# Kernel tuning notes

Hardware: AMD Instinct MI355X
Metric: run time of the kernel (lower is better)

The kernel has to match this reference:

```python
import jax, jax.numpy as jnp
import numpy as np


def _conv3x3(x, w, b):
    # x: [B,C,H,W], w: [O,C,3,3], b: [O]; stride 1, padding 1 (SAME)
    y = jax.lax.conv_general_dilated(
        x, w,
        window_strides=(1, 1),
        padding=((1, 1), (1, 1)),
        dimension_numbers=("NCHW", "OIHW", "NCHW"),
    )
    return y + b[None, :, None, None]


def setup_inputs() -> dict:
    key = jax.random.key(0)
    k_x, k_w1, k_b1, k_w2, k_b2 = jax.random.split(key, 5)
    B, Cin, H, W = 16, 128, 96, 96
    Ch = 256
    # Kaiming-ish small init for conv weights
    x = jax.random.normal(k_x, (B, Cin, H, W), dtype=jnp.float32)
    w1 = jax.random.normal(k_w1, (Ch, Cin, 3, 3), dtype=jnp.float32) * (1.0 / np.sqrt(Cin * 9))
    b1 = jax.random.normal(k_b1, (Ch,), dtype=jnp.float32) * 0.01
    w2 = jax.random.normal(k_w2, (2, Ch, 3, 3), dtype=jnp.float32) * (1.0 / np.sqrt(Ch * 9))
    b2 = jax.random.normal(k_b2, (2,), dtype=jnp.float32) * 0.01
    return {"x": x, "w1": w1, "b1": b1, "w2": w2, "b2": b2}


def reference(x, w1, b1, w2, b2):
    # DeformConv2d with zero offsets == plain 3x3 conv (stride 1, pad 1) + bias.
    h = jax.nn.relu(_conv3x3(x, w1, b1))  # [B,256,H,W]
    return _conv3x3(h, w2, b2)            # [B,2,H,W]
```

## Files before the change

### kernel.cpp

```cpp
#include <hip/hip_runtime.h>
#include <stdint.h>

typedef unsigned short ushort_t;
typedef __attribute__((ext_vector_type(8))) short short8;
typedef __attribute__((ext_vector_type(4))) float floatx4;
typedef __attribute__((ext_vector_type(4))) unsigned short ushortx4;
typedef __attribute__((ext_vector_type(8))) unsigned short ushortx8;

#define B_   16
#define CIN  128
#define CH   256
#define HW   96
#define HP   98

#define XPAD_ELEMS (B_*HP*HP*CIN)
#define HPAD_ELEMS (B_*HP*HP*CH)
#define XPAD_OFF 0
#define HPAD_OFF (XPAD_ELEMS*2)
#define W1T_OFF  (HPAD_OFF + HPAD_ELEMS*2)
#define W2T_OFF  (W1T_OFF + 256*1152*2)

__device__ __forceinline__ ushort_t f2bf(float f){
  uint32_t u = __float_as_uint(f);
  u += 0x7FFF + ((u >> 16) & 1);
  return (ushort_t)(u >> 16);
}
__device__ __forceinline__ float bf2f(ushort_t h){
  return __uint_as_float(((uint32_t)h) << 16);
}
__device__ __forceinline__ void async_ld16(void* lds, const void* g){
  __builtin_amdgcn_global_load_lds(
      (const __attribute__((address_space(1))) void*)g,
      (__attribute__((address_space(3))) void*)lds, 16, 0, 0);
}

__device__ __forceinline__ void zb(uint32_t* base, int C2, int tid){
  int perimg = 388*C2;
  int b = tid / perimg; int r = tid % perimg;
  int cell = r / C2;    int cu = r % C2;
  int y, x;
  if      (cell < 98)  { y = 0;            x = cell;       }
  else if (cell < 196) { y = 97;           x = cell - 98;  }
  else if (cell < 292) { y = cell - 195;   x = 0;          }
  else                 { y = cell - 291;   x = 97;         }
  base[((b*HP + y)*HP + x)*C2 + cu] = 0u;
}

__global__ __launch_bounds__(256) void prep_all(const float* __restrict__ x,
                                                const float* __restrict__ w1,
                                                const float* __restrict__ w2,
                                                uint32_t* __restrict__ xpadw,
                                                uint32_t* __restrict__ hpadw,
                                                ushort_t* __restrict__ w1t,
                                                float* __restrict__ w2t,
                                                ushort_t* __restrict__ xpad){
  __shared__ float lds[128][33];
  int bidx = blockIdx.x;
  int t = threadIdx.x;
  if (bidx < 4608){
    int xt = bidx % 3; int y = (bidx/3) % 96; int b = bidx/288;
    int x0 = xt*32;
    #pragma unroll
    for (int rep=0; rep<16; ++rep){
      int idx = rep*256 + t;
      int ci = idx >> 5, xj = idx & 31;
      lds[ci][xj] = x[((b*CIN + ci)*HW + y)*HW + x0 + xj];
    }
    __syncthreads();
    int px = t & 31, oc = t >> 5;
    ushort_t* dst = &xpad[((b*HP + y+1)*HP + x0+px+1)*CIN + oc*16];
    ushortx8 v0, v1;
    #pragma unroll
    for (int k=0;k<8;k++) v0[k] = f2bf(lds[oc*16+k][px]);
    #pragma unroll
    for (int k=0;k<8;k++) v1[k] = f2bf(lds[oc*16+8+k][px]);
    *(ushortx8*)dst = v0;
    *(ushortx8*)(dst+8) = v1;
  } else {
    int tid = (bidx - 4608)*256 + t;
    const int NZX = B_*388*64;
    const int NZH = B_*388*128;
    const int NW1 = 256*1152;
    if (tid < NZX){
      zb(xpadw, 64, tid);
    } else if (tid < NZX + NZH){
      zb(hpadw, 128, tid - NZX);
    } else if (tid < NZX + NZH + NW1){
      int r = tid - (NZX + NZH);
      int o = r / 1152, k = r - o*1152;
      int tap = k >> 7, c = k & 127;
      w1t[r] = f2bf(w1[(o*CIN + c)*9 + tap]);
    } else {
      int r = tid - (NZX + NZH + NW1);
      int ch = r & 1, c = (r >> 1) & 255, tap = r >> 9;
      w2t[r] = w2[(ch*CH + c)*9 + tap];
    }
  }
}

#define C1_TILE(KT, VMN, SA, SB) { \
  asm volatile("s_waitcnt vmcnt(" #VMN ")" ::: "memory"); \
  __builtin_amdgcn_s_barrier(); \
  __builtin_amdgcn_sched_barrier(0); \
  const int kt_ = (KT); \
  const ushort_t* Ab = &Alds[(kt_ & 1) * 16384]; \
  const ushort_t* Bb = &Blds[(kt_ % 3) * 12288]; \
  short8 a0[4], a1[4], b0[3], b1[3], b2[3], b3[3]; \
   \
  _Pragma("unroll") \
  for (int nf=0; nf<3; ++nf) b0[nf] = *(const short8*)&Bb[bbase_r + nf*1024 + koff0]; \
  _Pragma("unroll") \
  for (int mf=0; mf<4; ++mf) a0[mf] = *(const short8*)&Ab[abase_r + mf*1024 + koff0]; \
   \
  _Pragma("unroll") \
  for (int nf=0; nf<3; ++nf) b1[nf] = *(const short8*)&Bb[bbase_r + (nf+3)*1024 + koff0]; \
  if (SA) { \
    const int ka_ = kt_ + 1; const int ab_ = (ka_ & 1) * 16384; \
    async_ld16(&Alds[ab_ +     0 + adst], &w1t[asrc +       0 + ka_*64]); \
    async_ld16(&Alds[ab_ +  4096 + adst], &w1t[asrc +   73728 + ka_*64]); \
  } \
  __builtin_amdgcn_s_barrier(); \
  __builtin_amdgcn_sched_barrier(0); \
  __builtin_amdgcn_s_setprio(1); \
  _Pragma("unroll") \
  for (int mf=0; mf<4; ++mf) \
    _Pragma("unroll") \
    for (int nf=0; nf<3; ++nf) \
      acc[mf][nf] = __builtin_amdgcn_mfma_f32_16x16x32_bf16(a0[mf], b0[nf], acc[mf][nf], 0,0,0); \
  __builtin_amdgcn_s_setprio(0); \
  __builtin_amdgcn_s_barrier(); \
  __builtin_amdgcn_sched_barrier(0); \
   \
  _Pragma("unroll") \
  for (int mf=0; mf<4; ++mf) a1[mf] = *(const short8*)&Ab[abase_r + mf*1024 + koff1]; \
  _Pragma("unroll") \
  for (int nf=0; nf<3; ++nf) b2[nf] = *(const short8*)&Bb[bbase_r + nf*1024 + koff1]; \
  if (SA) { \
    const int ka_ = kt_ + 1; const int ab_ = (ka_ & 1) * 16384; \
    async_ld16(&Alds[ab_ +  8192 + adst], &w1t[asrc + 2*73728 + ka_*64]); \
    async_ld16(&Alds[ab_ + 12288 + adst], &w1t[asrc + 3*73728 + ka_*64]); \
  } \
  __builtin_amdgcn_s_barrier(); \
  __builtin_amdgcn_sched_barrier(0); \
  __builtin_amdgcn_s_setprio(1); \
  _Pragma("unroll") \
  for (int mf=0; mf<4; ++mf) \
    _Pragma("unroll") \
    for (int nf=0; nf<3; ++nf) \
      acc[mf][nf+3] = __builtin_amdgcn_mfma_f32_16x16x32_bf16(a0[mf], b1[nf], acc[mf][nf+3], 0,0,0); \
  __builtin_amdgcn_s_setprio(0); \
  __builtin_amdgcn_s_barrier(); \
  __builtin_amdgcn_sched_barrier(0); \
   \
  _Pragma("unroll") \
  for (int nf=0; nf<3; ++nf) b3[nf] = *(const short8*)&Bb[bbase_r + (nf+3)*1024 + koff1]; \
  if (SB) { \
    const int kb_ = kt_ + 2; \
    const int tapb_ = kb_ >> 1; \
    const int dyb_ = tapb_/3; const int dxb_ = tapb_ - dyb_*3; \
    const int bdb_ = (dyb_*HP + dxb_)*CIN + (kb_&1)*64; \
    const int bb_ = (kb_ % 3) * 12288; \
    async_ld16(&Blds[bb_ +    0 + bdst], &xpad[bsrc +            bdb_]); \
    async_ld16(&Blds[bb_ + 4096 + bdst], &xpad[bsrc + 2*HP*CIN + bdb_]); \
  } \
  __builtin_amdgcn_s_barrier(); \
  __builtin_amdgcn_sched_barrier(0); \
  __builtin_amdgcn_s_setprio(1); \
  _Pragma("unroll") \
  for (int mf=0; mf<4; ++mf) \
    _Pragma("unroll") \
    for (int nf=0; nf<3; ++nf) \
      acc[mf][nf] = __builtin_amdgcn_mfma_f32_16x16x32_bf16(a1[mf], b2[nf], acc[mf][nf], 0,0,0); \
  __builtin_amdgcn_s_setprio(0); \
  __builtin_amdgcn_s_barrier(); \
  __builtin_amdgcn_sched_barrier(0); \
   \
  if (SB) { \
    const int kb_ = kt_ + 2; \
    const int tapb_ = kb_ >> 1; \
    const int dyb_ = tapb_/3; const int dxb_ = tapb_ - dyb_*3; \
    const int bdb_ = (dyb_*HP + dxb_)*CIN + (kb_&1)*64; \
    const int bb_ = (kb_ % 3) * 12288; \
    async_ld16(&Blds[bb_ + 8192 + bdst], &xpad[bsrc + 4*HP*CIN + bdb_]); \
  } \
  __builtin_amdgcn_s_barrier(); \
  __builtin_amdgcn_sched_barrier(0); \
  __builtin_amdgcn_s_setprio(1); \
  _Pragma("unroll") \
  for (int mf=0; mf<4; ++mf) \
    _Pragma("unroll") \
    for (int nf=0; nf<3; ++nf) \
      acc[mf][nf+3] = __builtin_amdgcn_mfma_f32_16x16x32_bf16(a1[mf], b3[nf], acc[mf][nf+3], 0,0,0); \
  __builtin_amdgcn_s_setprio(0); \
}

__global__ __launch_bounds__(512, 1) void conv1(const ushort_t* __restrict__ xpad,
                                                const ushort_t* __restrict__ w1t,
                                                const float* __restrict__ b1,
                                                ushort_t* __restrict__ hpad){
  __shared__ __align__(16) ushort_t Alds[2*16384];
  __shared__ __align__(16) ushort_t Blds[3*12288];
  int orig = blockIdx.x;
  int bid = (orig & 7) * 96 + (orig >> 3);
  int b = bid / 48; int rem = bid - b*48;
  int y0 = (rem/3)*6, x0 = (rem - (rem/3)*3)*32;
  int t = threadIdx.x;
  int lane = t & 63, wave = t >> 6;
  int wm = wave & 3, wn = wave >> 2;
  int r = lane & 15, q = lane >> 4;

  const int arow0 = t >> 3;
  const int soct  = (t & 7) ^ (arow0 & 7);
  const int adst  = t * 8;
  const int asrc  = arow0 * 1152 + soct * 8;
  const int bty0  = arow0 >> 5, btx0 = arow0 & 31;
  const int bdst  = t * 8;
  const int bsrc  = ((b*HP + y0 + bty0)*HP + x0 + btx0)*CIN + soct * 8;

  const int koff0 = ((0*4 + q) ^ (r & 7)) * 8;
  const int koff1 = ((1*4 + q) ^ (r & 7)) * 8;
  const int abase_r = (wm*64 + r) * 64;
  const int bbase_r = (wn*96 + r) * 64;

  floatx4 acc[4][6];
  #pragma unroll
  for (int i=0;i<4;i++)
    #pragma unroll
    for (int j=0;j<6;j++) acc[i][j] = (floatx4){0.f,0.f,0.f,0.f};

  #pragma unroll
  for (int j=0;j<3;++j) async_ld16(&Blds[0     + j*4096 + bdst], &xpad[bsrc + j*(2*HP*CIN)]);
  #pragma unroll
  for (int j=0;j<4;++j) async_ld16(&Alds[0     + j*4096 + adst], &w1t[asrc + j*73728]);
  #pragma unroll
  for (int j=0;j<3;++j) async_ld16(&Blds[12288 + j*4096 + bdst], &xpad[bsrc + j*(2*HP*CIN) + 64]);

  for (int kt=0; kt<16; ++kt){
    C1_TILE(kt, 3, 1, 1)
  }
  C1_TILE(16, 3, 1, 0)
  C1_TILE(17, 0, 0, 0)

  #pragma unroll
  for (int mf=0; mf<4; ++mf){
    int o = wm*64 + mf*16 + q*4;
    float bias0 = b1[o], bias1 = b1[o+1], bias2 = b1[o+2], bias3 = b1[o+3];
    #pragma unroll
    for (int nf=0; nf<6; ++nf){
      int n = wn*96 + nf*16 + r;
      int ty = n >> 5, tx = n & 31;
      ushortx4 v;
      v[0] = f2bf(fmaxf(acc[mf][nf][0] + bias0, 0.f));
      v[1] = f2bf(fmaxf(acc[mf][nf][1] + bias1, 0.f));
      v[2] = f2bf(fmaxf(acc[mf][nf][2] + bias2, 0.f));
      v[3] = f2bf(fmaxf(acc[mf][nf][3] + bias3, 0.f));
      *(ushortx4*)&hpad[((b*HP + y0+ty+1)*HP + (x0+tx+1))*CH + o] = v;
    }
  }
}

__global__ __launch_bounds__(256) void conv2(const ushort_t* __restrict__ hpad,
                                             const float* __restrict__ w2t,
                                             const float* __restrict__ b2,
                                             float* __restrict__ out){
  __shared__ __align__(16) ushort_t hlds[25600];
  __shared__ float part[4][64][2];
  int bid = blockIdx.x;
  int b = bid / 144; int rem = bid - b*144;
  int yt = rem / 12, xt = rem - yt*12;
  int y0 = yt*8, x0 = xt*8;
  int t = threadIdx.x;
  int wave = t >> 6, lane = t & 63;

  for (int pass=0; pass<13; ++pass){
    int u = pass*256 + t;
    if (u < 3200){
      int cell = u >> 5, cf = u & 31;
      int hy = cell / 10, hx = cell - hy*10;
      const ushort_t* src = hpad + ((b*HP + y0+hy)*HP + (x0+hx))*CH
                                 + ((cf ^ (cell & 7)) << 3);
      async_ld16(&hlds[(pass*256 + wave*64)*8], src);
    }
  }
  __syncthreads();

  int q = __builtin_amdgcn_readfirstlane(wave);
  int ty = lane >> 3, tx = lane & 7;
  float a0 = 0.f, a1 = 0.f;
  for (int tap=0; tap<9; ++tap){
    int dy = tap/3, dxx = tap - dy*3;
    int cell = (ty+dy)*10 + (tx+dxx);
    int s = cell & 7;
    const float* wp = w2t + (tap*256 + q*64)*2;
    #pragma unroll
    for (int g=0; g<8; ++g){
      int j = q*8 + g;
      ushortx8 hv = *(const ushortx8*)&hlds[cell*256 + ((j ^ s) << 3)];
      #pragma unroll
      for (int i=0;i<8;i++){
        float hf = bf2f(hv[i]);
        a0 = fmaf(hf, wp[(g*8+i)*2    ], a0);
        a1 = fmaf(hf, wp[(g*8+i)*2 + 1], a1);
      }
    }
  }
  part[wave][lane][0] = a0;
  part[wave][lane][1] = a1;
  __syncthreads();
  if (t < 128){
    int sel = t >> 6, pix = t & 63;
    float v = part[0][pix][sel] + part[1][pix][sel]
            + part[2][pix][sel] + part[3][pix][sel] + b2[sel];
    int yy = y0 + (pix >> 3), xx = x0 + (pix & 7);
    out[(b*2 + sel)*9216 + yy*96 + xx] = v;
  }
}

extern "C" void kernel_launch(void* const* d_in, const int* in_sizes, int n_in,
                              void* d_out, int out_size, void* d_ws, size_t ws_size,
                              hipStream_t stream){
  const float* x  = (const float*)d_in[0];
  const float* w1 = (const float*)d_in[1];
  const float* b1 = (const float*)d_in[2];
  const float* w2 = (const float*)d_in[3];
  const float* b2 = (const float*)d_in[4];
  float* out = (float*)d_out;
  char* ws = (char*)d_ws;
  ushort_t* xpad = (ushort_t*)(ws + XPAD_OFF);
  ushort_t* hpad = (ushort_t*)(ws + HPAD_OFF);
  ushort_t* w1t  = (ushort_t*)(ws + W1T_OFF);
  float*    w2t  = (float*)(ws + W2T_OFF);

  hipLaunchKernelGGL(prep_all, dim3(10434), dim3(256), 0, stream,
                     x, w1, w2, (uint32_t*)xpad, (uint32_t*)hpad, w1t, w2t, xpad);
  hipLaunchKernelGGL(conv1, dim3(768),  dim3(512), 0, stream, xpad, w1t, b1, hpad);
  hipLaunchKernelGGL(conv2, dim3(2304), dim3(256), 0, stream, hpad, w2t, b2, out);
}
```

Measured before the change: 157.9 us.

## Halve conv1 block to 4 waves with 128x96 per-wave tiles

The conv1 block shrinks from 8 waves to 4, and each wave now computes a 128x96 output tile (8x6 MFMA accumulators) instead of 64x96. Each thread issues twice as many async loads per stage, and the wait counts are raised to match. A and B fragments are reused across more MFMAs, cutting LDS read traffic per FLOP. The cost is much higher register pressure from 192 accumulator floats per lane and only 4 waves per CU to hide latency, since launch_bounds is (256,1).

Measured after the change: 169.6 us. 1.07x slower.

```diff
diff --git a/kernel.cpp b/kernel.cpp
--- a/kernel.cpp
+++ b/kernel.cpp
@@ -105,55 +105,66 @@
   const int kt_ = (KT); \
   const ushort_t* Ab = &Alds[(kt_ & 1) * 16384]; \
   const ushort_t* Bb = &Blds[(kt_ % 3) * 12288]; \
-  short8 a0[4], a1[4], b0[3], b1[3], b2[3], b3[3]; \
+  short8 aA[4], aB[4], bA[3], bB[3]; \
    \
   _Pragma("unroll") \
-  for (int nf=0; nf<3; ++nf) b0[nf] = *(const short8*)&Bb[bbase_r + nf*1024 + koff0]; \
-  _Pragma("unroll") \
-  for (int mf=0; mf<4; ++mf) a0[mf] = *(const short8*)&Ab[abase_r + mf*1024 + koff0]; \
-   \
-  _Pragma("unroll") \
-  for (int nf=0; nf<3; ++nf) b1[nf] = *(const short8*)&Bb[bbase_r + (nf+3)*1024 + koff0]; \
+  for (int nf=0; nf<3; ++nf) bA[nf] = *(const short8*)&Bb[bbase_r + nf*1024 + koff0]; \
+  _Pragma("unroll") \
+  for (int nf=0; nf<3; ++nf) bB[nf] = *(const short8*)&Bb[bbase_r + (nf+3)*1024 + koff0]; \
+  _Pragma("unroll") \
+  for (int mf=0; mf<4; ++mf) aA[mf] = *(const short8*)&Ab[abase_r + mf*1024 + koff0]; \
   if (SA) { \
     const int ka_ = kt_ + 1; const int ab_ = (ka_ & 1) * 16384; \
-    async_ld16(&Alds[ab_ +     0 + adst], &w1t[asrc +       0 + ka_*64]); \
-    async_ld16(&Alds[ab_ +  4096 + adst], &w1t[asrc +   73728 + ka_*64]); \
+    async_ld16(&Alds[ab_ +    0 + adst], &w1t[asrc +       0 + ka_*64]); \
+    async_ld16(&Alds[ab_ + 2048 + adst], &w1t[asrc +   36864 + ka_*64]); \
+    async_ld16(&Alds[ab_ + 4096 + adst], &w1t[asrc + 2*36864 + ka_*64]); \
+    async_ld16(&Alds[ab_ + 6144 + adst], &w1t[asrc + 3*36864 + ka_*64]); \
   } \
   __builtin_amdgcn_s_barrier(); \
   __builtin_amdgcn_sched_barrier(0); \
   __builtin_amdgcn_s_setprio(1); \
   _Pragma("unroll") \
-  for (int mf=0; mf<4; ++mf) \
+  for (int mf=0; mf<4; ++mf){ \
     _Pragma("unroll") \
-    for (int nf=0; nf<3; ++nf) \
-      acc[mf][nf] = __builtin_amdgcn_mfma_f32_16x16x32_bf16(a0[mf], b0[nf], acc[mf][nf], 0,0,0); \
+    for (int nf=0; nf<3; ++nf){ \
+      acc[mf][nf]   = __builtin_amdgcn_mfma_f32_16x16x32_bf16(aA[mf], bA[nf], acc[mf][nf],   0,0,0); \
+      acc[mf][nf+3] = __builtin_amdgcn_mfma_f32_16x16x32_bf16(aA[mf], bB[nf], acc[mf][nf+3], 0,0,0); \
+    } \
+  } \
   __builtin_amdgcn_s_setprio(0); \
   __builtin_amdgcn_s_barrier(); \
   __builtin_amdgcn_sched_barrier(0); \
    \
   _Pragma("unroll") \
-  for (int mf=0; mf<4; ++mf) a1[mf] = *(const short8*)&Ab[abase_r + mf*1024 + koff1]; \
-  _Pragma("unroll") \
-  for (int nf=0; nf<3; ++nf) b2[nf] = *(const short8*)&Bb[bbase_r + nf*1024 + koff1]; \
+  for (int mf=0; mf<4; ++mf) aB[mf] = *(const short8*)&Ab[abase_r + (mf+4)*1024 + koff0]; \
   if (SA) { \
     const int ka_ = kt_ + 1; const int ab_ = (ka_ & 1) * 16384; \
-    async_ld16(&Alds[ab_ +  8192 + adst], &w1t[asrc + 2*73728 + ka_*64]); \
-    async_ld16(&Alds[ab_ + 12288 + adst], &w1t[asrc + 3*73728 + ka_*64]); \
+    async_ld16(&Alds[ab_ +  8192 + adst], &w1t[asrc + 4*36864 + ka_*64]); \
+    async_ld16(&Alds[ab_ + 10240 + adst], &w1t[asrc + 5*36864 + ka_*64]); \
+    async_ld16(&Alds[ab_ + 12288 + adst], &w1t[asrc + 6*36864 + ka_*64]); \
+    async_ld16(&Alds[ab_ + 14336 + adst], &w1t[asrc + 7*36864 + ka_*64]); \
   } \
   __builtin_amdgcn_s_barrier(); \
   __builtin_amdgcn_sched_barrier(0); \
   __builtin_amdgcn_s_setprio(1); \
   _Pragma("unroll") \
-  for (int mf=0; mf<4; ++mf) \
+  for (int mf=0; mf<4; ++mf){ \
     _Pragma("unroll") \
-    for (int nf=0; nf<3; ++nf) \
-      acc[mf][nf+3] = __builtin_amdgcn_mfma_f32_16x16x32_bf16(a0[mf], b1[nf], acc[mf][nf+3], 0,0,0); \
+    for (int nf=0; nf<3; ++nf){ \
+      acc[mf+4][nf]   = __builtin_amdgcn_mfma_f32_16x16x32_bf16(aB[mf], bA[nf], acc[mf+4][nf],   0,0,0); \
+      acc[mf+4][nf+3] = __builtin_amdgcn_mfma_f32_16x16x32_bf16(aB[mf], bB[nf], acc[mf+4][nf+3], 0,0,0); \
+    } \
+  } \
   __builtin_amdgcn_s_setprio(0); \
   __builtin_amdgcn_s_barrier(); \
   __builtin_amdgcn_sched_barrier(0); \
    \
   _Pragma("unroll") \
-  for (int nf=0; nf<3; ++nf) b3[nf] = *(const short8*)&Bb[bbase_r + (nf+3)*1024 + koff1]; \
+  for (int nf=0; nf<3; ++nf) bA[nf] = *(const short8*)&Bb[bbase_r + nf*1024 + koff1]; \
+  _Pragma("unroll") \
+  for (int nf=0; nf<3; ++nf) bB[nf] = *(const short8*)&Bb[bbase_r + (nf+3)*1024 + koff1]; \
+  _Pragma("unroll") \
+  for (int mf=0; mf<4; ++mf) aA[mf] = *(const short8*)&Ab[abase_r + mf*1024 + koff1]; \
   if (SB) { \
     const int kb_ = kt_ + 2; \
     const int tapb_ = kb_ >> 1; \
@@ -161,40 +172,51 @@
     const int bdb_ = (dyb_*HP + dxb_)*CIN + (kb_&1)*64; \
     const int bb_ = (kb_ % 3) * 12288; \
     async_ld16(&Blds[bb_ +    0 + bdst], &xpad[bsrc +            bdb_]); \
+    async_ld16(&Blds[bb_ + 2048 + bdst], &xpad[bsrc +   HP*CIN + bdb_]); \
     async_ld16(&Blds[bb_ + 4096 + bdst], &xpad[bsrc + 2*HP*CIN + bdb_]); \
   } \
   __builtin_amdgcn_s_barrier(); \
   __builtin_amdgcn_sched_barrier(0); \
   __builtin_amdgcn_s_setprio(1); \
   _Pragma("unroll") \
-  for (int mf=0; mf<4; ++mf) \
+  for (int mf=0; mf<4; ++mf){ \
     _Pragma("unroll") \
-    for (int nf=0; nf<3; ++nf) \
-      acc[mf][nf] = __builtin_amdgcn_mfma_f32_16x16x32_bf16(a1[mf], b2[nf], acc[mf][nf], 0,0,0); \
+    for (int nf=0; nf<3; ++nf){ \
+      acc[mf][nf]   = __builtin_amdgcn_mfma_f32_16x16x32_bf16(aA[mf], bA[nf], acc[mf][nf],   0,0,0); \
+      acc[mf][nf+3] = __builtin_amdgcn_mfma_f32_16x16x32_bf16(aA[mf], bB[nf], acc[mf][nf+3], 0,0,0); \
+    } \
+  } \
   __builtin_amdgcn_s_setprio(0); \
   __builtin_amdgcn_s_barrier(); \
   __builtin_amdgcn_sched_barrier(0); \
    \
+  _Pragma("unroll") \
+  for (int mf=0; mf<4; ++mf) aB[mf] = *(const short8*)&Ab[abase_r + (mf+4)*1024 + koff1]; \
   if (SB) { \
     const int kb_ = kt_ + 2; \
     const int tapb_ = kb_ >> 1; \
     const int dyb_ = tapb_/3; const int dxb_ = tapb_ - dyb_*3; \
     const int bdb_ = (dyb_*HP + dxb_)*CIN + (kb_&1)*64; \
     const int bb_ = (kb_ % 3) * 12288; \
-    async_ld16(&Blds[bb_ + 8192 + bdst], &xpad[bsrc + 4*HP*CIN + bdb_]); \
+    async_ld16(&Blds[bb_ +  6144 + bdst], &xpad[bsrc + 3*HP*CIN + bdb_]); \
+    async_ld16(&Blds[bb_ +  8192 + bdst], &xpad[bsrc + 4*HP*CIN + bdb_]); \
+    async_ld16(&Blds[bb_ + 10240 + bdst], &xpad[bsrc + 5*HP*CIN + bdb_]); \
   } \
   __builtin_amdgcn_s_barrier(); \
   __builtin_amdgcn_sched_barrier(0); \
   __builtin_amdgcn_s_setprio(1); \
   _Pragma("unroll") \
-  for (int mf=0; mf<4; ++mf) \
+  for (int mf=0; mf<4; ++mf){ \
     _Pragma("unroll") \
-    for (int nf=0; nf<3; ++nf) \
-      acc[mf][nf+3] = __builtin_amdgcn_mfma_f32_16x16x32_bf16(a1[mf], b3[nf], acc[mf][nf+3], 0,0,0); \
+    for (int nf=0; nf<3; ++nf){ \
+      acc[mf+4][nf]   = __builtin_amdgcn_mfma_f32_16x16x32_bf16(aB[mf], bA[nf], acc[mf+4][nf],   0,0,0); \
+      acc[mf+4][nf+3] = __builtin_amdgcn_mfma_f32_16x16x32_bf16(aB[mf], bB[nf], acc[mf+4][nf+3], 0,0,0); \
+    } \
+  } \
   __builtin_amdgcn_s_setprio(0); \
 }
 
-__global__ __launch_bounds__(512, 1) void conv1(const ushort_t* __restrict__ xpad,
+__global__ __launch_bounds__(256, 1) void conv1(const ushort_t* __restrict__ xpad,
                                                 const ushort_t* __restrict__ w1t,
                                                 const float* __restrict__ b1,
                                                 ushort_t* __restrict__ hpad){
@@ -206,44 +228,43 @@
   int y0 = (rem/3)*6, x0 = (rem - (rem/3)*3)*32;
   int t = threadIdx.x;
   int lane = t & 63, wave = t >> 6;
-  int wm = wave & 3, wn = wave >> 2;
+  int wm = wave & 1, wn = wave >> 1;
   int r = lane & 15, q = lane >> 4;
 
   const int arow0 = t >> 3;
   const int soct  = (t & 7) ^ (arow0 & 7);
   const int adst  = t * 8;
   const int asrc  = arow0 * 1152 + soct * 8;
-  const int bty0  = arow0 >> 5, btx0 = arow0 & 31;
   const int bdst  = t * 8;
-  const int bsrc  = ((b*HP + y0 + bty0)*HP + x0 + btx0)*CIN + soct * 8;
+  const int bsrc  = ((b*HP + y0)*HP + x0 + arow0)*CIN + soct * 8;
 
   const int koff0 = ((0*4 + q) ^ (r & 7)) * 8;
   const int koff1 = ((1*4 + q) ^ (r & 7)) * 8;
-  const int abase_r = (wm*64 + r) * 64;
-  const int bbase_r = (wn*96 + r) * 64;
-
-  floatx4 acc[4][6];
-  #pragma unroll
-  for (int i=0;i<4;i++)
+  const int abase_r = (wm*128 + r) * 64;
+  const int bbase_r = (wn*96  + r) * 64;
+
+  floatx4 acc[8][6];
+  #pragma unroll
+  for (int i=0;i<8;i++)
     #pragma unroll
     for (int j=0;j<6;j++) acc[i][j] = (floatx4){0.f,0.f,0.f,0.f};
 
   #pragma unroll
-  for (int j=0;j<3;++j) async_ld16(&Blds[0     + j*4096 + bdst], &xpad[bsrc + j*(2*HP*CIN)]);
-  #pragma unroll
-  for (int j=0;j<4;++j) async_ld16(&Alds[0     + j*4096 + adst], &w1t[asrc + j*73728]);
-  #pragma unroll
-  for (int j=0;j<3;++j) async_ld16(&Blds[12288 + j*4096 + bdst], &xpad[bsrc + j*(2*HP*CIN) + 64]);
+  for (int j=0;j<6;++j) async_ld16(&Blds[0     + j*2048 + bdst], &xpad[bsrc + j*HP*CIN]);
+  #pragma unroll
+  for (int j=0;j<8;++j) async_ld16(&Alds[0     + j*2048 + adst], &w1t[asrc + j*36864]);
+  #pragma unroll
+  for (int j=0;j<6;++j) async_ld16(&Blds[12288 + j*2048 + bdst], &xpad[bsrc + j*HP*CIN + 64]);
 
   for (int kt=0; kt<16; ++kt){
-    C1_TILE(kt, 3, 1, 1)
-  }
-  C1_TILE(16, 3, 1, 0)
+    C1_TILE(kt, 6, 1, 1)
+  }
+  C1_TILE(16, 6, 1, 0)
   C1_TILE(17, 0, 0, 0)
 
   #pragma unroll
-  for (int mf=0; mf<4; ++mf){
-    int o = wm*64 + mf*16 + q*4;
+  for (int mf=0; mf<8; ++mf){
+    int o = wm*128 + mf*16 + q*4;
     float bias0 = b1[o], bias1 = b1[o+1], bias2 = b1[o+2], bias3 = b1[o+3];
     #pragma unroll
     for (int nf=0; nf<6; ++nf){
@@ -333,6 +354,6 @@
 
   hipLaunchKernelGGL(prep_all, dim3(10434), dim3(256), 0, stream,
                      x, w1, w2, (uint32_t*)xpad, (uint32_t*)hpad, w1t, w2t, xpad);
-  hipLaunchKernelGGL(conv1, dim3(768),  dim3(512), 0, stream, xpad, w1t, b1, hpad);
+  hipLaunchKernelGGL(conv1, dim3(768),  dim3(256), 0, stream, xpad, w1t, b1, hpad);
   hipLaunchKernelGGL(conv2, dim3(2304), dim3(256), 0, stream, hpad, w2t, b2, out);
 }
```

## Stage input halo window in LDS once instead of streaming per-tap B tiles

Applied to the files above, without the earlier changes.

Conv1 now loads the whole padded input halo (8x34 pixels by 128 channels, row stride padded to 136) into LDS once at the start, and reads each tap's B fragments directly from that window by offset. This replaces the triple-buffered per-tap B streaming from global memory, which re-fetched the overlapping halo nine times. It removes redundant global and LDS traffic for the input. In exchange, the prologue is a synchronous bulk load, the pipeline now waits with vmcnt(0) and lgkmcnt(0) each tile, and LDS use grows, which may add stalls or bank conflicts.

Result: slower. 161.3 us (+2.2%).

```diff
diff --git a/kernel.cpp b/kernel.cpp
--- a/kernel.cpp
+++ b/kernel.cpp
@@ -98,99 +98,87 @@
   }
 }
 
-#define C1_TILE(KT, VMN, SA, SB) { \
-  asm volatile("s_waitcnt vmcnt(" #VMN ")" ::: "memory"); \
+#define C1_TILE(KT, SA) { \
+  asm volatile("s_waitcnt vmcnt(0)" ::: "memory"); \
   __builtin_amdgcn_s_barrier(); \
   __builtin_amdgcn_sched_barrier(0); \
   const int kt_ = (KT); \
   const ushort_t* Ab = &Alds[(kt_ & 1) * 16384]; \
-  const ushort_t* Bb = &Blds[(kt_ % 3) * 12288]; \
-  short8 a0[4], a1[4], b0[3], b1[3], b2[3], b3[3]; \
+  const int tap_ = (KT) >> 1; \
+  const int dy_ = tap_ / 3, dx_ = tap_ - dy_*3; \
+  const int dt_ = (dy_*34 + dx_)*136 + ((KT)&1)*64;    \
+  short8 aA[4], bA[3], bB[3]; \
    \
   _Pragma("unroll") \
-  for (int nf=0; nf<3; ++nf) b0[nf] = *(const short8*)&Bb[bbase_r + nf*1024 + koff0]; \
-  _Pragma("unroll") \
-  for (int mf=0; mf<4; ++mf) a0[mf] = *(const short8*)&Ab[abase_r + mf*1024 + koff0]; \
-   \
-  _Pragma("unroll") \
-  for (int nf=0; nf<3; ++nf) b1[nf] = *(const short8*)&Bb[bbase_r + (nf+3)*1024 + koff0]; \
+  for (int nf=0; nf<3; ++nf) bA[nf] = *(const short8*)&Wlds[cb136[nf] + q8 + dt_]; \
+  _Pragma("unroll") \
+  for (int mf=0; mf<4; ++mf) aA[mf] = *(const short8*)&Ab[abase_r + mf*1024 + koff0]; \
   if (SA) { \
     const int ka_ = kt_ + 1; const int ab_ = (ka_ & 1) * 16384; \
-    async_ld16(&Alds[ab_ +     0 + adst], &w1t[asrc +       0 + ka_*64]); \
-    async_ld16(&Alds[ab_ +  4096 + adst], &w1t[asrc +   73728 + ka_*64]); \
+    async_ld16(&Alds[ab_ +    0 + adst], &w1t[asrc +       0 + ka_*64]); \
+    async_ld16(&Alds[ab_ + 4096 + adst], &w1t[asrc +   73728 + ka_*64]); \
   } \
   __builtin_amdgcn_s_barrier(); \
+  asm volatile("s_waitcnt lgkmcnt(0)" ::: "memory"); \
   __builtin_amdgcn_sched_barrier(0); \
   __builtin_amdgcn_s_setprio(1); \
   _Pragma("unroll") \
   for (int mf=0; mf<4; ++mf) \
     _Pragma("unroll") \
     for (int nf=0; nf<3; ++nf) \
-      acc[mf][nf] = __builtin_amdgcn_mfma_f32_16x16x32_bf16(a0[mf], b0[nf], acc[mf][nf], 0,0,0); \
+      acc[mf][nf] = __builtin_amdgcn_mfma_f32_16x16x32_bf16(aA[mf], bA[nf], acc[mf][nf], 0,0,0); \
   __builtin_amdgcn_s_setprio(0); \
   __builtin_amdgcn_s_barrier(); \
   __builtin_amdgcn_sched_barrier(0); \
    \
   _Pragma("unroll") \
-  for (int mf=0; mf<4; ++mf) a1[mf] = *(const short8*)&Ab[abase_r + mf*1024 + koff1]; \
-  _Pragma("unroll") \
-  for (int nf=0; nf<3; ++nf) b2[nf] = *(const short8*)&Bb[bbase_r + nf*1024 + koff1]; \
+  for (int nf=0; nf<3; ++nf) bB[nf] = *(const short8*)&Wlds[cb136[nf+3] + q8 + dt_]; \
   if (SA) { \
     const int ka_ = kt_ + 1; const int ab_ = (ka_ & 1) * 16384; \
     async_ld16(&Alds[ab_ +  8192 + adst], &w1t[asrc + 2*73728 + ka_*64]); \
     async_ld16(&Alds[ab_ + 12288 + adst], &w1t[asrc + 3*73728 + ka_*64]); \
   } \
   __builtin_amdgcn_s_barrier(); \
+  asm volatile("s_waitcnt lgkmcnt(0)" ::: "memory"); \
   __builtin_amdgcn_sched_barrier(0); \
   __builtin_amdgcn_s_setprio(1); \
   _Pragma("unroll") \
   for (int mf=0; mf<4; ++mf) \
     _Pragma("unroll") \
     for (int nf=0; nf<3; ++nf) \
-      acc[mf][nf+3] = __builtin_amdgcn_mfma_f32_16x16x32_bf16(a0[mf], b1[nf], acc[mf][nf+3], 0,0,0); \
+      acc[mf][nf+3] = __builtin_amdgcn_mfma_f32_16x16x32_bf16(aA[mf], bB[nf], acc[mf][nf+3], 0,0,0); \
   __builtin_amdgcn_s_setprio(0); \
   __builtin_amdgcn_s_barrier(); \
   __builtin_amdgcn_sched_barrier(0); \
    \
   _Pragma("unroll") \
-  for (int nf=0; nf<3; ++nf) b3[nf] = *(const short8*)&Bb[bbase_r + (nf+3)*1024 + koff1]; \
-  if (SB) { \
-    const int kb_ = kt_ + 2; \
-    const int tapb_ = kb_ >> 1; \
-    const int dyb_ = tapb_/3; const int dxb_ = tapb_ - dyb_*3; \
-    const int bdb_ = (dyb_*HP + dxb_)*CIN + (kb_&1)*64; \
-    const int bb_ = (kb_ % 3) * 12288; \
-    async_ld16(&Blds[bb_ +    0 + bdst], &xpad[bsrc +            bdb_]); \
-    async_ld16(&Blds[bb_ + 4096 + bdst], &xpad[bsrc + 2*HP*CIN + bdb_]); \
-  } \
-  __builtin_amdgcn_s_barrier(); \
+  for (int nf=0; nf<3; ++nf) bA[nf] = *(const short8*)&Wlds[cb136[nf] + q8 + dt_ + 32]; \
+  _Pragma("unroll") \
+  for (int mf=0; mf<4; ++mf) aA[mf] = *(const short8*)&Ab[abase_r + mf*1024 + koff1]; \
+  __builtin_amdgcn_s_barrier(); \
+  asm volatile("s_waitcnt lgkmcnt(0)" ::: "memory"); \
   __builtin_amdgcn_sched_barrier(0); \
   __builtin_amdgcn_s_setprio(1); \
   _Pragma("unroll") \
   for (int mf=0; mf<4; ++mf) \
     _Pragma("unroll") \
     for (int nf=0; nf<3; ++nf) \
-      acc[mf][nf] = __builtin_amdgcn_mfma_f32_16x16x32_bf16(a1[mf], b2[nf], acc[mf][nf], 0,0,0); \
+      acc[mf][nf] = __builtin_amdgcn_mfma_f32_16x16x32_bf16(aA[mf], bA[nf], acc[mf][nf], 0,0,0); \
   __builtin_amdgcn_s_setprio(0); \
   __builtin_amdgcn_s_barrier(); \
   __builtin_amdgcn_sched_barrier(0); \
    \
-  if (SB) { \
-    const int kb_ = kt_ + 2; \
-    const int tapb_ = kb_ >> 1; \
-    const int dyb_ = tapb_/3; const int dxb_ = tapb_ - dyb_*3; \
-    const int bdb_ = (dyb_*HP + dxb_)*CIN + (kb_&1)*64; \
-    const int bb_ = (kb_ % 3) * 12288; \
-    async_ld16(&Blds[bb_ + 8192 + bdst], &xpad[bsrc + 4*HP*CIN + bdb_]); \
-  } \
-  __builtin_amdgcn_s_barrier(); \
+  _Pragma("unroll") \
+  for (int nf=0; nf<3; ++nf) bB[nf] = *(const short8*)&Wlds[cb136[nf+3] + q8 + dt_ + 32]; \
+  __builtin_amdgcn_s_barrier(); \
+  asm volatile("s_waitcnt lgkmcnt(0)" ::: "memory"); \
   __builtin_amdgcn_sched_barrier(0); \
   __builtin_amdgcn_s_setprio(1); \
   _Pragma("unroll") \
   for (int mf=0; mf<4; ++mf) \
     _Pragma("unroll") \
     for (int nf=0; nf<3; ++nf) \
-      acc[mf][nf+3] = __builtin_amdgcn_mfma_f32_16x16x32_bf16(a1[mf], b3[nf], acc[mf][nf+3], 0,0,0); \
+      acc[mf][nf+3] = __builtin_amdgcn_mfma_f32_16x16x32_bf16(aA[mf], bB[nf], acc[mf][nf+3], 0,0,0); \
   __builtin_amdgcn_s_setprio(0); \
 }
 
@@ -199,7 +187,7 @@
                                                 const float* __restrict__ b1,
                                                 ushort_t* __restrict__ hpad){
   __shared__ __align__(16) ushort_t Alds[2*16384];
-  __shared__ __align__(16) ushort_t Blds[3*12288];
+  __shared__ __align__(16) ushort_t Wlds[272*136];
   int orig = blockIdx.x;
   int bid = (orig & 7) * 96 + (orig >> 3);
   int b = bid / 48; int rem = bid - b*48;
@@ -213,14 +201,18 @@
   const int soct  = (t & 7) ^ (arow0 & 7);
   const int adst  = t * 8;
   const int asrc  = arow0 * 1152 + soct * 8;
-  const int bty0  = arow0 >> 5, btx0 = arow0 & 31;
-  const int bdst  = t * 8;
-  const int bsrc  = ((b*HP + y0 + bty0)*HP + x0 + btx0)*CIN + soct * 8;
 
   const int koff0 = ((0*4 + q) ^ (r & 7)) * 8;
   const int koff1 = ((1*4 + q) ^ (r & 7)) * 8;
   const int abase_r = (wm*64 + r) * 64;
-  const int bbase_r = (wn*96 + r) * 64;
+
+  const int q8 = q * 8;
+  int cb136[6];
+  #pragma unroll
+  for (int nf=0; nf<6; ++nf){
+    int n = wn*96 + nf*16 + r;
+    cb136[nf] = ((n >> 5)*34 + (n & 31)) * 136;
+  }
 
   floatx4 acc[4][6];
   #pragma unroll
@@ -228,18 +220,24 @@
     #pragma unroll
     for (int j=0;j<6;j++) acc[i][j] = (floatx4){0.f,0.f,0.f,0.f};
 
+  for (int p=0; p<9; ++p){
+    int u = p*512 + t;
+    if (u < 4352){
+      int cell = u >> 4, oct = u & 15;
+      int cy = cell / 34, cx = cell - cy*34;
+      ushortx8 v = *(const ushortx8*)&xpad[((b*HP + y0 + cy)*HP + x0 + cx)*CIN + oct*8];
+      *(ushortx8*)&Wlds[cell*136 + oct*8] = v;
+    }
+  }
   #pragma unroll
-  for (int j=0;j<3;++j) async_ld16(&Blds[0     + j*4096 + bdst], &xpad[bsrc + j*(2*HP*CIN)]);
-  #pragma unroll
-  for (int j=0;j<4;++j) async_ld16(&Alds[0     + j*4096 + adst], &w1t[asrc + j*73728]);
-  #pragma unroll
-  for (int j=0;j<3;++j) async_ld16(&Blds[12288 + j*4096 + bdst], &xpad[bsrc + j*(2*HP*CIN) + 64]);
-
-  for (int kt=0; kt<16; ++kt){
-    C1_TILE(kt, 3, 1, 1)
-  }
-  C1_TILE(16, 3, 1, 0)
-  C1_TILE(17, 0, 0, 0)
+  for (int j=0;j<4;++j) async_ld16(&Alds[j*4096 + adst], &w1t[asrc + j*73728]);
+  __syncthreads();
+
+  C1_TILE(0, 1)  C1_TILE(1, 1)  C1_TILE(2, 1)  C1_TILE(3, 1)
+  C1_TILE(4, 1)  C1_TILE(5, 1)  C1_TILE(6, 1)  C1_TILE(7, 1)
+  C1_TILE(8, 1)  C1_TILE(9, 1)  C1_TILE(10, 1) C1_TILE(11, 1)
+  C1_TILE(12, 1) C1_TILE(13, 1) C1_TILE(14, 1) C1_TILE(15, 1)
+  C1_TILE(16, 1) C1_TILE(17, 0)
 
   #pragma unroll
   for (int mf=0; mf<4; ++mf){
```
